# Optimization experiments

Measured on AMD Instinct MI355X. Metric: run time of the kernel, lower is better.

The kernel has to match this reference:

```python
import jax, jax.numpy as jnp
import numpy as np

EPS = 1e-7  # K.epsilon()


def setup_inputs() -> dict:
    key = jax.random.key(0)
    k1, k2, k3 = jax.random.split(key, 3)
    B, H, W, Cin, Cout, KH, KW = 8, 128, 128, 256, 256, 3, 3
    x = jax.random.normal(k1, (B, H, W, Cin), dtype=jnp.float32)
    style = jax.random.normal(k2, (B, Cin), dtype=jnp.float32)
    # he_uniform-ish scale for the kernel
    fan_in = KH * KW * Cin
    limit = np.sqrt(6.0 / fan_in)
    kernel = jax.random.uniform(k3, (KH, KW, Cin, Cout), dtype=jnp.float32,
                                minval=-limit, maxval=limit)
    return {"x": x, "style": style, "kernel": kernel}


def reference(x, style, kernel):
    # Demodulation factor: rsqrt(sum_{kh,kw,cin} (kernel * style)^2 + eps), shape (B, Cout).
    # Equivalent to the original's broadcast-then-reduce, computed without
    # materializing the (B,kh,kw,Cin,Cout) modulated weight tensor.
    k2 = jnp.sum(jnp.square(kernel), axis=(0, 1))          # (Cin, Cout)
    ssq = jnp.einsum('io,bi->bo', k2, jnp.square(style))   # (B, Cout)
    demod = jax.lax.rsqrt(ssq + EPS)                       # (B, Cout)

    # Modulate input per-sample, then shared-weight conv (same padding, stride 1).
    xm = x * style[:, None, None, :]                       # (B,H,W,Cin)
    y = jax.lax.conv_general_dilated(
        xm, kernel,
        window_strides=(1, 1), padding='SAME',
        dimension_numbers=('NHWC', 'HWIO', 'NHWC'))
    return y * demod[:, None, None, :]
```

## Files before the change

### kernel.cpp

```cpp
#include <hip/hip_runtime.h>
#include <hip/hip_bf16.h>
#include <stdint.h>

typedef short short8 __attribute__((ext_vector_type(8)));
typedef float f32x4 __attribute__((ext_vector_type(4)));

#define KKTOT 2304
#define PXS   40

__device__ __forceinline__ short f2bf(float f) {
    __hip_bfloat16 h = __float2bfloat16(f);
    return __builtin_bit_cast(short, h);
}

__global__ void prep_k2(const float* __restrict__ kern, float* __restrict__ K2)
{
    const int ci = blockIdx.x, co = threadIdx.x;
    float acc = 0.f;
#pragma unroll
    for (int p = 0; p < 9; ++p) {
        float w = kern[(p * 256 + ci) * 256 + co];
        acc += w * w;
    }
    K2[ci * 256 + co] = acc;
}

__global__ void prep_demod(const float* __restrict__ style,
                           const float* __restrict__ K2,
                           float* __restrict__ demod)
{
    const int b = blockIdx.x, co = threadIdx.x;
    __shared__ float s2[256];
    float s = style[b * 256 + co];
    s2[co] = s * s;
    __syncthreads();
    float acc = 0.f;
#pragma unroll 8
    for (int ci = 0; ci < 256; ++ci)
        acc += s2[ci] * K2[ci * 256 + co];
    demod[b * 256 + co] = 1.0f / sqrtf(acc + 1e-7f);
}

__global__ void prep_kt(const float* __restrict__ kern,
                        __hip_bfloat16* __restrict__ kT)
{
    __shared__ float tile[64][65];
    const int t   = threadIdx.x;
    const int k0  = blockIdx.x << 6;
    const int c0  = blockIdx.y << 6;
    const int col = t & 63;
    const int rb  = (t >> 6) << 4;
#pragma unroll
    for (int r = 0; r < 16; ++r) {
        int kl = rb + r;
        tile[kl][col] = kern[(size_t)(k0 + kl) * 256 + c0 + col];
    }
    __syncthreads();
#pragma unroll
    for (int r = 0; r < 16; ++r) {
        int co = rb + r;
        kT[(size_t)(c0 + co) * KKTOT + k0 + col] = __float2bfloat16(tile[col][co]);
    }
}

__global__ __launch_bounds__(256) void conv_mfma(
    const float* __restrict__ x,
    const __hip_bfloat16* __restrict__ kt,
    const float* __restrict__ style,
    const float* __restrict__ demod,
    float* __restrict__ out)
{
    __shared__ __align__(16) __hip_bfloat16 Xs[130 * PXS];
    __shared__ __align__(16) __hip_bfloat16 Bs[3 * 128 * PXS];
    __shared__ float Ss[256];
    __shared__ float Ds[128];

    const int t    = threadIdx.x;
    const int bid  = blockIdx.x;
    const int L    = ((bid & 7) << 8) | (bid >> 3);
    const int n0   = (L & 1) << 7;
    const int bh   = L >> 1;
    const int b    = bh >> 7, h = bh & 127;
    const int wave = t >> 6, lane = t & 63;
    const int wr   = (wave >> 1) << 6;
    const int wc   = (wave & 1) << 6;
    const int l15  = lane & 15, lk = lane >> 4;
    const int mA   = t >> 2;
    const int koff = (t & 3) << 3;

    if (t < 128) {
        ((float2*)Ss)[t] = ((const float2*)(style + b * 256))[t];
        Ds[t] = demod[b * 256 + n0 + t];
    }
    if (t < 32) {
        Xs[t]             = __float2bfloat16(0.f);
        Xs[129 * PXS + t] = __float2bfloat16(0.f);
    }

    f32x4 acc[4][4] = {};

    for (int sl = 0; sl < 24; ++sl) {
        const int h2 = h + (sl >> 3) - 1;
        if ((unsigned)h2 >= 128u) continue;
        const int ci0     = (sl & 7) << 5;
        const int posbase = (sl >> 3) * 3;

        __syncthreads();

        const size_t rowbase = (size_t)(b * 128 + h2) * 128;
        const float* ga = x + (rowbase + mA)      * 256 + ci0 + koff;
        const float* gb = x + (rowbase + mA + 64) * 256 + ci0 + koff;
        float4 xa0 = *(const float4*)ga,       xa1 = *(const float4*)(ga + 4);
        float4 xb0 = *(const float4*)gb,       xb1 = *(const float4*)(gb + 4);
        float4 s0  = *(const float4*)&Ss[ci0 + koff];
        float4 s1  = *(const float4*)&Ss[ci0 + koff + 4];
        short8 ma, mb;
#pragma unroll
        for (int jj = 0; jj < 4; ++jj) {
            ma[jj]     = f2bf((&xa0.x)[jj] * (&s0.x)[jj]);
            ma[jj + 4] = f2bf((&xa1.x)[jj] * (&s1.x)[jj]);
            mb[jj]     = f2bf((&xb0.x)[jj] * (&s0.x)[jj]);
            mb[jj + 4] = f2bf((&xb1.x)[jj] * (&s1.x)[jj]);
        }
        *(short8*)&Xs[(mA + 1)  * PXS + koff] = ma;
        *(short8*)&Xs[(mA + 65) * PXS + koff] = mb;

        const __hip_bfloat16* gw =
            kt + (size_t)(n0 + mA) * KKTOT + posbase * 256 + ci0 + koff;
#pragma unroll
        for (int tp = 0; tp < 3; ++tp) {
            short8 w0 = *(const short8*)(gw + tp * 256);
            short8 w1 = *(const short8*)(gw + tp * 256 + 64 * KKTOT);
            *(short8*)&Bs[tp * (128 * PXS) + mA * PXS + koff]        = w0;
            *(short8*)&Bs[tp * (128 * PXS) + (mA + 64) * PXS + koff] = w1;
        }
        __syncthreads();

#pragma unroll
        for (int tp = 0; tp < 3; ++tp) {
            short8 af[4], bfr[4];
#pragma unroll
            for (int i = 0; i < 4; ++i)
                af[i] = *(const short8*)&Xs[(wr + i * 16 + l15 + tp) * PXS + lk * 8];
#pragma unroll
            for (int j = 0; j < 4; ++j)
                bfr[j] = *(const short8*)&Bs[tp * (128 * PXS) + (wc + j * 16 + l15) * PXS + lk * 8];
#pragma unroll
            for (int i = 0; i < 4; ++i)
#pragma unroll
                for (int j = 0; j < 4; ++j)
                    acc[i][j] = __builtin_amdgcn_mfma_f32_16x16x32_bf16(
                        af[i], bfr[j], acc[i][j], 0, 0, 0);
        }
    }

    float dj[4];
#pragma unroll
    for (int j = 0; j < 4; ++j) dj[j] = Ds[wc + j * 16 + l15];
    const size_t obase = (size_t)(b * 128 + h) * 128 * 256 + n0;
#pragma unroll
    for (int i = 0; i < 4; ++i) {
#pragma unroll
        for (int j = 0; j < 4; ++j) {
            const int n = wc + j * 16 + l15;
#pragma unroll
            for (int r = 0; r < 4; ++r) {
                const int m = wr + i * 16 + lk * 4 + r;
                out[obase + (size_t)m * 256 + n] = acc[i][j][r] * dj[j];
            }
        }
    }
}

extern "C" void kernel_launch(void* const* d_in, const int* in_sizes, int n_in,
                              void* d_out, int out_size, void* d_ws, size_t ws_size,
                              hipStream_t stream)
{
    const float* x     = (const float*)d_in[0];
    const float* style = (const float*)d_in[1];
    const float* kern  = (const float*)d_in[2];
    float* out = (float*)d_out;

    char*  ws    = (char*)d_ws;
    float* demod = (float*)ws;
    float* K2    = (float*)(ws + 8192);
    __hip_bfloat16* kT = (__hip_bfloat16*)(ws + 270336);

    prep_k2   <<<256, 256, 0, stream>>>(kern, K2);
    prep_demod<<<8,   256, 0, stream>>>(style, K2, demod);
    prep_kt   <<<dim3(36, 4), 256, 0, stream>>>(kern, kT);
    conv_mfma <<<2048, 256, 0, stream>>>(x, kT, style, demod, out);
}
```

Baseline: 353.0 us.

## Prepack weights in MFMA fragment order and double-buffer input tiles

Weights are pre-permuted into a per-lane MFMA fragment layout, so each wave reads its B operands straight from global/L2 memory instead of staging them through shared memory. The input row tile is double-buffered in LDS, with the next slice's global loads issued before the current MFMAs. This drops one of the two barriers per slice. The out-of-range h rows are now skipped through loop bounds rather than a continue. The trade-off is that each wave now fetches weight fragments from global memory on every slice, so performance depends on those reads hitting in cache, and the extra LDS buffer adds to shared-memory use.

```diff
diff --git a/kernel.cpp b/kernel.cpp
--- a/kernel.cpp
+++ b/kernel.cpp
@@ -5,8 +5,7 @@
 typedef short short8 __attribute__((ext_vector_type(8)));
 typedef float f32x4 __attribute__((ext_vector_type(4)));
 
-#define KKTOT 2304
-#define PXS   40
+#define PXS 40
 
 __device__ __forceinline__ short f2bf(float f) {
     __hip_bfloat16 h = __float2bfloat16(f);
@@ -41,37 +40,37 @@
     demod[b * 256 + co] = 1.0f / sqrtf(acc + 1e-7f);
 }
 
-__global__ void prep_kt(const float* __restrict__ kern,
-                        __hip_bfloat16* __restrict__ kT)
-{
-    __shared__ float tile[64][65];
-    const int t   = threadIdx.x;
-    const int k0  = blockIdx.x << 6;
-    const int c0  = blockIdx.y << 6;
-    const int col = t & 63;
-    const int rb  = (t >> 6) << 4;
-#pragma unroll
-    for (int r = 0; r < 16; ++r) {
-        int kl = rb + r;
-        tile[kl][col] = kern[(size_t)(k0 + kl) * 256 + c0 + col];
-    }
-    __syncthreads();
-#pragma unroll
-    for (int r = 0; r < 16; ++r) {
-        int co = rb + r;
-        kT[(size_t)(c0 + co) * KKTOT + k0 + col] = __float2bfloat16(tile[col][co]);
+__global__ void prep_kf(const float* __restrict__ kern,
+                        __hip_bfloat16* __restrict__ kf)
+{
+    const int st = blockIdx.x;
+    const int sl = st / 3, tp = st - sl * 3;
+    const int dh = sl >> 3, cc = sl & 7;
+    const int p  = dh * 3 + tp;
+    const int t    = threadIdx.x;
+    const int lane = t & 63, jt2 = t >> 6;
+    const int l15  = lane & 15, lk = lane >> 4;
+    const int cib  = cc * 32 + lk * 8;
+#pragma unroll
+    for (int jj = 0; jj < 4; ++jj) {
+        const int jt = jj * 4 + jt2;
+        const int co = jt * 16 + l15;
+        short8 v;
+#pragma unroll
+        for (int e = 0; e < 8; ++e)
+            v[e] = f2bf(kern[(size_t)(p * 256 + cib + e) * 256 + co]);
+        *(short8*)(kf + ((size_t)(st * 16 + jt) * 64 + lane) * 8) = v;
     }
 }
 
 __global__ __launch_bounds__(256) void conv_mfma(
     const float* __restrict__ x,
-    const __hip_bfloat16* __restrict__ kt,
+    const __hip_bfloat16* __restrict__ kf,
     const float* __restrict__ style,
     const float* __restrict__ demod,
     float* __restrict__ out)
 {
-    __shared__ __align__(16) __hip_bfloat16 Xs[130 * PXS];
-    __shared__ __align__(16) __hip_bfloat16 Bs[3 * 128 * PXS];
+    __shared__ __align__(16) __hip_bfloat16 Xs[2][130 * PXS];
     __shared__ float Ss[256];
     __shared__ float Ds[128];
 
@@ -87,31 +86,33 @@
     const int l15  = lane & 15, lk = lane >> 4;
     const int mA   = t >> 2;
     const int koff = (t & 3) << 3;
+    const int jbase = ((L & 1) << 3) + (wc >> 4);
 
     if (t < 128) {
         ((float2*)Ss)[t] = ((const float2*)(style + b * 256))[t];
         Ds[t] = demod[b * 256 + n0 + t];
     }
     if (t < 32) {
-        Xs[t]             = __float2bfloat16(0.f);
-        Xs[129 * PXS + t] = __float2bfloat16(0.f);
+        const __hip_bfloat16 z = __float2bfloat16(0.f);
+        Xs[0][t] = z; Xs[0][129 * PXS + t] = z;
+        Xs[1][t] = z; Xs[1][129 * PXS + t] = z;
     }
 
     f32x4 acc[4][4] = {};
 
-    for (int sl = 0; sl < 24; ++sl) {
-        const int h2 = h + (sl >> 3) - 1;
-        if ((unsigned)h2 >= 128u) continue;
-        const int ci0     = (sl & 7) << 5;
-        const int posbase = (sl >> 3) * 3;
-
-        __syncthreads();
-
+    const int slo = (h == 0)   ? 8  : 0;
+    const int shi = (h == 127) ? 16 : 24;
+
+    __syncthreads();
+
+    {
+        const int h2  = h + (slo >> 3) - 1;
+        const int ci0 = (slo & 7) << 5;
         const size_t rowbase = (size_t)(b * 128 + h2) * 128;
         const float* ga = x + (rowbase + mA)      * 256 + ci0 + koff;
         const float* gb = x + (rowbase + mA + 64) * 256 + ci0 + koff;
-        float4 xa0 = *(const float4*)ga,       xa1 = *(const float4*)(ga + 4);
-        float4 xb0 = *(const float4*)gb,       xb1 = *(const float4*)(gb + 4);
+        float4 xa0 = *(const float4*)ga, xa1 = *(const float4*)(ga + 4);
+        float4 xb0 = *(const float4*)gb, xb1 = *(const float4*)(gb + 4);
         float4 s0  = *(const float4*)&Ss[ci0 + koff];
         float4 s1  = *(const float4*)&Ss[ci0 + koff + 4];
         short8 ma, mb;
@@ -122,29 +123,38 @@
             mb[jj]     = f2bf((&xb0.x)[jj] * (&s0.x)[jj]);
             mb[jj + 4] = f2bf((&xb1.x)[jj] * (&s1.x)[jj]);
         }
-        *(short8*)&Xs[(mA + 1)  * PXS + koff] = ma;
-        *(short8*)&Xs[(mA + 65) * PXS + koff] = mb;
-
-        const __hip_bfloat16* gw =
-            kt + (size_t)(n0 + mA) * KKTOT + posbase * 256 + ci0 + koff;
+        *(short8*)&Xs[0][(mA + 1)  * PXS + koff] = ma;
+        *(short8*)&Xs[0][(mA + 65) * PXS + koff] = mb;
+    }
+    __syncthreads();
+
+    int cur = 0;
+    for (int s = slo; s < shi; ++s, cur ^= 1) {
+        float4 xa0, xa1, xb0, xb1;
+        int nci0 = 0;
+        const bool pf = (s + 1 < shi);
+        if (pf) {
+            const int sl = s + 1;
+            const int h2 = h + (sl >> 3) - 1;
+            nci0 = (sl & 7) << 5;
+            const size_t rowbase = (size_t)(b * 128 + h2) * 128;
+            const float* ga = x + (rowbase + mA)      * 256 + nci0 + koff;
+            const float* gb = x + (rowbase + mA + 64) * 256 + nci0 + koff;
+            xa0 = *(const float4*)ga; xa1 = *(const float4*)(ga + 4);
+            xb0 = *(const float4*)gb; xb1 = *(const float4*)(gb + 4);
+        }
+
+        const size_t stbase = (size_t)s * 3 * 16;
 #pragma unroll
         for (int tp = 0; tp < 3; ++tp) {
-            short8 w0 = *(const short8*)(gw + tp * 256);
-            short8 w1 = *(const short8*)(gw + tp * 256 + 64 * KKTOT);
-            *(short8*)&Bs[tp * (128 * PXS) + mA * PXS + koff]        = w0;
-            *(short8*)&Bs[tp * (128 * PXS) + (mA + 64) * PXS + koff] = w1;
-        }
-        __syncthreads();
-
-#pragma unroll
-        for (int tp = 0; tp < 3; ++tp) {
-            short8 af[4], bfr[4];
+            short8 bfr[4], af[4];
+#pragma unroll
+            for (int j = 0; j < 4; ++j)
+                bfr[j] = *(const short8*)(kf +
+                    (((stbase + tp * 16) + jbase + j) * 64 + lane) * 8);
 #pragma unroll
             for (int i = 0; i < 4; ++i)
-                af[i] = *(const short8*)&Xs[(wr + i * 16 + l15 + tp) * PXS + lk * 8];
-#pragma unroll
-            for (int j = 0; j < 4; ++j)
-                bfr[j] = *(const short8*)&Bs[tp * (128 * PXS) + (wc + j * 16 + l15) * PXS + lk * 8];
+                af[i] = *(const short8*)&Xs[cur][(wr + i * 16 + l15 + tp) * PXS + lk * 8];
 #pragma unroll
             for (int i = 0; i < 4; ++i)
 #pragma unroll
@@ -152,6 +162,22 @@
                     acc[i][j] = __builtin_amdgcn_mfma_f32_16x16x32_bf16(
                         af[i], bfr[j], acc[i][j], 0, 0, 0);
         }
+
+        if (pf) {
+            float4 s0 = *(const float4*)&Ss[nci0 + koff];
+            float4 s1 = *(const float4*)&Ss[nci0 + koff + 4];
+            short8 ma, mb;
+#pragma unroll
+            for (int jj = 0; jj < 4; ++jj) {
+                ma[jj]     = f2bf((&xa0.x)[jj] * (&s0.x)[jj]);
+                ma[jj + 4] = f2bf((&xa1.x)[jj] * (&s1.x)[jj]);
+                mb[jj]     = f2bf((&xb0.x)[jj] * (&s0.x)[jj]);
+                mb[jj + 4] = f2bf((&xb1.x)[jj] * (&s1.x)[jj]);
+            }
+            *(short8*)&Xs[cur ^ 1][(mA + 1)  * PXS + koff] = ma;
+            *(short8*)&Xs[cur ^ 1][(mA + 65) * PXS + koff] = mb;
+        }
+        __syncthreads();
     }
 
     float dj[4];
@@ -188,6 +214,6 @@
 
     prep_k2   <<<256, 256, 0, stream>>>(kern, K2);
     prep_demod<<<8,   256, 0, stream>>>(style, K2, demod);
-    prep_kt   <<<dim3(36, 4), 256, 0, stream>>>(kern, kT);
+    prep_kf   <<<72,  256, 0, stream>>>(kern, kT);
     conv_mfma <<<2048, 256, 0, stream>>>(x, kT, style, demod, out);
 }
```

Measured after the change: 368.9 us. 4.5% more time.
